# Optimization experiments

Hardware: AMD Instinct MI355X
Metric: run time of the kernel (lower is better)

## Reference

```python
import jax, jax.numpy as jnp
import numpy as np
from jax import lax

WSIZE = 11
SIGMA = 1.5
PAD = WSIZE // 2  # 5
C1 = 0.01 ** 2
C2 = 0.03 ** 2


def _gauss1d():
    x = np.arange(WSIZE) - WSIZE // 2
    g = np.exp(-(x.astype(np.float64) ** 2) / (2.0 * SIGMA ** 2))
    g = g / g.sum()
    return jnp.asarray(g, dtype=jnp.float32)


def _blur3d(x, g):
    """Replicate-pad by 5 on D/H/W then apply the separable 11x11x11 Gaussian.
    x: [N, 1, D, H, W]. Mathematically identical to the dense conv3d in the
    original (the 3D window is an exact outer product of the 1D Gaussian)."""
    xp = jnp.pad(x, ((0, 0), (0, 0), (PAD, PAD), (PAD, PAD), (PAD, PAD)), mode='edge')
    dn = ('NCDHW', 'OIDHW', 'NCDHW')
    for kshape in ((1, 1, WSIZE, 1, 1), (1, 1, 1, WSIZE, 1), (1, 1, 1, 1, WSIZE)):
        xp = lax.conv_general_dilated(xp, g.reshape(kshape), (1, 1, 1), 'VALID',
                                      dimension_numbers=dn)
    return xp


def _rerange(img):
    img = jnp.where(img.max() > 128.0, img / 255.0, img)
    img = jnp.where(img.min() < -0.5, (img + 1.0) / 2.0, img)
    return img


def setup_inputs() -> dict:
    key = jax.random.key(0)
    k1, k2 = jax.random.split(key)
    N, C, H, W = 4, 16, 512, 512
    pred = jax.random.uniform(k1, (N, C, H, W), dtype=jnp.float32)
    gt = jax.random.uniform(k2, (N, C, H, W), dtype=jnp.float32)
    return {"pred": pred, "gt": gt}


def reference(pred, gt):
    N = pred.shape[0]
    pred = _rerange(pred)
    gt = _rerange(gt)

    # ---- PSNR (range = 1.0, reduce='sum') ----
    mse = jnp.mean((pred - gt) ** 2, axis=(1, 2, 3))           # [N]
    psnr = jnp.sum(10.0 * jnp.log10(1.0 / mse))                # scalar

    # ---- 3D SSIM over [N,1,C,H,W] volumes ----
    g = _gauss1d()
    img = pred[:, None]                                        # [N,1,D,H,W]
    gtt = gt[:, None]
    mu1 = _blur3d(img, g)
    mu2 = _blur3d(gtt, g)
    mu1_sq = mu1 * mu1
    mu2_sq = mu2 * mu2
    mu1_mu2 = mu1 * mu2
    sigma1_sq = _blur3d(img * img, g) - mu1_sq
    sigma2_sq = _blur3d(gtt * gtt, g) - mu2_sq
    sigma12 = _blur3d(img * gtt, g) - mu1_mu2

    v1 = 2.0 * sigma12 + C2
    v2 = sigma1_sq + sigma2_sq + C2
    ssim_map = ((2.0 * mu1_mu2 + C1) * v1) / ((mu1_sq + mu2_sq + C1) * v2)
    ssim = jnp.sum(jnp.mean(ssim_map, axis=(1, 2, 3, 4)))      # reduce='sum'

    return psnr, ssim, N
```

## Files before the change

kernel.cpp:

```cpp
#include <hip/hip_runtime.h>
#include <hip/hip_bf16.h>
#include <cmath>


#define NB 4
#define DD 16
#define HH 512
#define WW 512
#define SLICE (HH * WW)
#define VOL (DD * SLICE)
#define C1F 0.0001f
#define C2F 0.0009f

#define TH 16
#define TW 32
#define SH 26
#define SW 42
#define ST 43
#define NTHR 512
#define NIT 3

struct GW { float g[11]; };

__device__ inline float blo(unsigned v) {
  union { unsigned u; float f; } c; c.u = v << 16; return c.f;
}
__device__ inline float bhi(unsigned v) {
  union { unsigned u; float f; } c; c.u = v & 0xFFFF0000u; return c.f;
}
__device__ inline unsigned pack_bf2(float a, float b) {
  __hip_bfloat162 t;
  t.x = __float2bfloat16(a);
  t.y = __float2bfloat16(b);
  union { __hip_bfloat162 h; unsigned u; } c; c.h = t; return c.u;
}

__device__ inline float block_sum512(float v) {
#pragma unroll
  for (int o = 32; o > 0; o >>= 1) v += __shfl_down(v, o, 64);
  __shared__ float r[8];
  if ((threadIdx.x & 63) == 0) r[threadIdx.x >> 6] = v;
  __syncthreads();
  float out = 0.f;
  if (threadIdx.x == 0) {
#pragma unroll
    for (int i = 0; i < 8; ++i) out += r[i];
  }
  __syncthreads();
  return out;
}

__global__ void zero_acc_k(float* acc) {
  if (threadIdx.x < 8) acc[threadIdx.x] = 0.f;
}

__global__ __launch_bounds__(NTHR, 2) void fused_k(
    const float* __restrict__ pred, const float* __restrict__ gt,
    float* __restrict__ acc, GW gw) {
  __shared__ uint2 sd[2][SH * ST];
  __shared__ uint2 tmp[TH * ST];
  __shared__ float WL[DD * DD];
  int b = blockIdx.x;
  int tile = b & 511;
  int n = b >> 9;
  int th0 = (tile >> 4) * TH;
  int tw0 = (tile & 15) * TW;
  int t = threadIdx.x;

  if (t < DD * DD) {
    int dout = t >> 4, d = t & 15;
    float w = 0.f;
#pragma unroll
    for (int k = 0; k < 11; ++k) {
      int j = dout + k - 5; j = j < 0 ? 0 : (j > 15 ? 15 : j);
      if (j == d) w += gw.g[k];
    }
    WL[t] = w;
  }

  int goff[NIT], laddr[NIT];
  bool iv[NIT], own[NIT];
#pragma unroll
  for (int it = 0; it < NIT; ++it) {
    int i = t + it * NTHR;
    iv[it] = i < SH * SW;
    int ii = iv[it] ? i : 0;
    int y = ii / SW, x = ii - y * SW;
    int gy = th0 + y - 5; gy = gy < 0 ? 0 : (gy > HH - 1 ? HH - 1 : gy);
    int gx = tw0 + x - 5; gx = gx < 0 ? 0 : (gx > WW - 1 ? WW - 1 : gx);
    goff[it] = gy * WW + gx;
    laddr[it] = y * ST + x;
    own[it] = (y >= 5) && (y < 5 + TH) && (x >= 5) && (x < 5 + TW);
  }
  const float* pbase = pred + (size_t)n * VOL;
  const float* qbase = gt + (size_t)n * VOL;

  float pv[NIT], qv[NIT];
#pragma unroll
  for (int it = 0; it < NIT; ++it) {
    pv[it] = iv[it] ? pbase[goff[it]] : 0.f;
    qv[it] = iv[it] ? qbase[goff[it]] : 0.f;
  }

  float psnr = 0.f;
  float a0[DD], a1[DD], a2[DD], a3[DD];
#pragma unroll
  for (int j = 0; j < DD; ++j) { a0[j] = a1[j] = a2[j] = a3[j] = 0.f; }
  __syncthreads();

  int wy = t >> 5, wx = t & 31;
#pragma unroll 1
  for (int d = 0; d < DD; ++d) {
    uint2* sdb = sd[d & 1];
#pragma unroll
    for (int it = 0; it < NIT; ++it) {
      if (iv[it]) {
        float S = pv[it] + qv[it], Dm = pv[it] - qv[it];
        sdb[laddr[it]] = make_uint2(pack_bf2(S, Dm), pack_bf2(S * S, Dm * Dm));
        if (own[it]) psnr = fmaf(Dm, Dm, psnr);
      }
    }
    __syncthreads();
    if (d < DD - 1) {
      const float* pd = pbase + (size_t)(d + 1) * SLICE;
      const float* qd = qbase + (size_t)(d + 1) * SLICE;
#pragma unroll
      for (int it = 0; it < NIT; ++it) {
        if (iv[it]) { pv[it] = pd[goff[it]]; qv[it] = qd[goff[it]]; }
      }
    }
    for (int i = t; i < TH * SW; i += NTHR) {
      int r = i / SW, c = i - r * SW;
      float h0 = 0.f, h1 = 0.f, h2 = 0.f, h3 = 0.f;
#pragma unroll
      for (int k = 0; k < 11; ++k) {
        uint2 v = sdb[(r + k) * ST + c];
        float g = gw.g[k];
        h0 = fmaf(g, blo(v.x), h0);
        h1 = fmaf(g, bhi(v.x), h1);
        h2 = fmaf(g, blo(v.y), h2);
        h3 = fmaf(g, bhi(v.y), h3);
      }
      tmp[r * ST + c] = make_uint2(pack_bf2(h0, h1), pack_bf2(h2, h3));
    }
    __syncthreads();
    float w0 = 0.f, w1 = 0.f, w2 = 0.f, w3 = 0.f;
#pragma unroll
    for (int k = 0; k < 11; ++k) {
      uint2 v = tmp[wy * ST + wx + k];
      float g = gw.g[k];
      w0 = fmaf(g, blo(v.x), w0);
      w1 = fmaf(g, bhi(v.x), w1);
      w2 = fmaf(g, blo(v.y), w2);
      w3 = fmaf(g, bhi(v.y), w3);
    }
    const float* wl = WL + d;
#pragma unroll
    for (int dout = 0; dout < DD; ++dout) {
      float w = wl[dout * DD];
      a0[dout] = fmaf(w, w0, a0[dout]);
      a1[dout] = fmaf(w, w1, a1[dout]);
      a2[dout] = fmaf(w, w2, a2[dout]);
      a3[dout] = fmaf(w, w3, a3[dout]);
    }
  }

  float ssum = 0.f;
#pragma unroll
  for (int j = 0; j < DD; ++j) {
    float Sb = a0[j], Db = a1[j], B1 = a2[j], B2 = a3[j];
    float SS = Sb * Sb, DDm = Db * Db;
    float m12_2 = (SS - DDm) * 0.5f;
    float msq   = (SS + DDm) * 0.5f;
    float Epq   = (B1 - B2) * 0.25f;
    float Esum  = (B1 + B2) * 0.5f;
    float sig12_2 = 2.f * Epq - m12_2;
    float svar    = Esum - msq;
    float num = (m12_2 + C1F) * (sig12_2 + C2F);
    float den = (msq + C1F) * (svar + C2F);
    ssum += num / den;
  }
  float bs = block_sum512(ssum);
  if (t == 0) atomicAdd(&acc[4 + n], bs);
  float bp = block_sum512(psnr);
  if (t == 0) atomicAdd(&acc[n], bp);
}

__global__ void final_k(const float* __restrict__ acc, float* __restrict__ out) {
  if (threadIdx.x == 0 && blockIdx.x == 0) {
    double psnr = 0.0, ssim = 0.0;
    for (int n = 0; n < NB; ++n) {
      double mse = (double)acc[n] / (double)VOL;
      psnr += 10.0 * log10(1.0 / mse);
      ssim += (double)acc[4 + n] / (double)VOL;
    }
    out[0] = (float)psnr;
    out[1] = (float)ssim;
    out[2] = (float)NB;
  }
}

extern "C" void kernel_launch(void* const* d_in, const int* in_sizes, int n_in,
                              void* d_out, int out_size, void* d_ws, size_t ws_size,
                              hipStream_t stream) {
  const float* pred = (const float*)d_in[0];
  const float* gt = (const float*)d_in[1];
  float* acc = (float*)d_ws;
  GW gw;
  double tt[11], s = 0.0;
  for (int i = 0; i < 11; ++i) {
    double x = i - 5;
    tt[i] = exp(-(x * x) / 4.5);
    s += tt[i];
  }
  for (int i = 0; i < 11; ++i) gw.g[i] = (float)(tt[i] / s);

  zero_acc_k<<<1, 64, 0, stream>>>(acc);
  fused_k<<<NB * 512, NTHR, 0, stream>>>(pred, gt, acc, gw);
  final_k<<<1, 1, 0, stream>>>(acc, (float*)d_out);
}
```

Baseline: 273.3 us.

## Use packed fp16 dot2 for separable blur with row/column-pair LDS layout

Switches the intermediate blur data from bf16 to fp16 and replaces the scalar FMA taps with v_dot2 instructions over packed pairs of taps. The shared memory is relaid so each word holds two adjacent rows or columns, and the weights are pre-packed on the host as even/odd-phase half2 constants. The depth-mixing weight matrix moves into kernel arguments, which removes the per-block shared-memory setup. The aim is to halve the ALU work and LDS reads in the H and W passes. The cost is fp16 range and precision for the squared terms and more complex indexing.

```diff
diff --git a/kernel.cpp b/kernel.cpp
--- a/kernel.cpp
+++ b/kernel.cpp
@@ -1,5 +1,4 @@
 #include <hip/hip_runtime.h>
-#include <hip/hip_bf16.h>
 #include <cmath>
 
 
@@ -14,25 +13,37 @@
 
 #define TH 16
 #define TW 32
-#define SH 26
 #define SW 42
-#define ST 43
+#define RP 13
+#define CP 21
+#define CPP 22
+#define CPT 22
 #define NTHR 512
-#define NIT 3
-
-struct GW { float g[11]; };
-
-__device__ inline float blo(unsigned v) {
-  union { unsigned u; float f; } c; c.u = v << 16; return c.f;
-}
-__device__ inline float bhi(unsigned v) {
-  union { unsigned u; float f; } c; c.u = v & 0xFFFF0000u; return c.f;
-}
-__device__ inline unsigned pack_bf2(float a, float b) {
-  __hip_bfloat162 t;
-  t.x = __float2bfloat16(a);
-  t.y = __float2bfloat16(b);
-  union { __hip_bfloat162 h; unsigned u; } c; c.h = t; return c.u;
+#define SIT (RP * SW)
+#define HIT (TH * CP)
+#define XTRA (SIT - NTHR)
+
+typedef _Float16 h2v __attribute__((ext_vector_type(2)));
+
+struct KArg {
+  float wlT[DD * DD];
+  unsigned ge[6], go[6];
+};
+
+__device__ inline float dot2h(unsigned a, unsigned b, float c) {
+#if __has_builtin(__builtin_amdgcn_fdot2)
+  return __builtin_amdgcn_fdot2(__builtin_bit_cast(h2v, a),
+                                __builtin_bit_cast(h2v, b), c, false);
+#else
+  h2v av = __builtin_bit_cast(h2v, a), bv = __builtin_bit_cast(h2v, b);
+  return fmaf((float)av.y, (float)bv.y, fmaf((float)av.x, (float)bv.x, c));
+#endif
+}
+__device__ inline unsigned pkh(float a, float b) {
+  return __builtin_bit_cast(unsigned, __builtin_amdgcn_cvt_pkrtz(a, b));
+}
+__device__ inline int iclamp(int v, int lo, int hi) {
+  return v < lo ? lo : (v > hi ? hi : v);
 }
 
 __device__ inline float block_sum512(float v) {
@@ -56,10 +67,12 @@
 
 __global__ __launch_bounds__(NTHR, 2) void fused_k(
     const float* __restrict__ pred, const float* __restrict__ gt,
-    float* __restrict__ acc, GW gw) {
-  __shared__ uint2 sd[2][SH * ST];
-  __shared__ uint2 tmp[TH * ST];
-  __shared__ float WL[DD * DD];
+    float* __restrict__ acc, KArg ka) {
+  __shared__ uint2 sA[2][RP * 2 * CPP];
+  __shared__ uint2 sB[2][RP * 2 * CPP];
+  __shared__ uint2 tA[TH * CPT];
+  __shared__ uint2 tB[TH * CPT];
+
   int b = blockIdx.x;
   int tile = b & 511;
   int n = b >> 9;
@@ -67,97 +80,121 @@
   int tw0 = (tile & 15) * TW;
   int t = threadIdx.x;
 
-  if (t < DD * DD) {
-    int dout = t >> 4, d = t & 15;
-    float w = 0.f;
-#pragma unroll
-    for (int k = 0; k < 11; ++k) {
-      int j = dout + k - 5; j = j < 0 ? 0 : (j > 15 ? 15 : j);
-      if (j == d) w += gw.g[k];
-    }
-    WL[t] = w;
-  }
-
-  int goff[NIT], laddr[NIT];
-  bool iv[NIT], own[NIT];
-#pragma unroll
-  for (int it = 0; it < NIT; ++it) {
-    int i = t + it * NTHR;
-    iv[it] = i < SH * SW;
-    int ii = iv[it] ? i : 0;
-    int y = ii / SW, x = ii - y * SW;
-    int gy = th0 + y - 5; gy = gy < 0 ? 0 : (gy > HH - 1 ? HH - 1 : gy);
-    int gx = tw0 + x - 5; gx = gx < 0 ? 0 : (gx > WW - 1 ? WW - 1 : gx);
-    goff[it] = gy * WW + gx;
-    laddr[it] = y * ST + x;
-    own[it] = (y >= 5) && (y < 5 + TH) && (x >= 5) && (x < 5 + TW);
-  }
-  const float* pbase = pred + (size_t)n * VOL;
-  const float* qbase = gt + (size_t)n * VOL;
-
-  float pv[NIT], qv[NIT];
-#pragma unroll
-  for (int it = 0; it < NIT; ++it) {
-    pv[it] = iv[it] ? pbase[goff[it]] : 0.f;
-    qv[it] = iv[it] ? qbase[goff[it]] : 0.f;
-  }
+  int rpA = t / SW, xA = t - rpA * SW;
+  int r0A = th0 + 2 * rpA - 5;
+  int gxA = iclamp(tw0 + xA - 5, 0, WW - 1);
+  int go00 = iclamp(r0A, 0, HH - 1) * WW + gxA;
+  int go01 = iclamp(r0A + 1, 0, HH - 1) * WW + gxA;
+  int wof0 = (rpA * 2 + (xA & 1)) * CPP + (xA >> 1);
+  bool oxA = (xA >= 5) && (xA < 5 + TW);
+  float o00 = (oxA && rpA >= 3 && rpA <= 10) ? 1.f : 0.f;
+  float o01 = (oxA && rpA >= 2 && rpA <= 9) ? 1.f : 0.f;
+
+  int i1 = t + XTRA;
+  bool has2 = (i1 >= NTHR);
+  int rpB = i1 / SW, xB = i1 - rpB * SW;
+  int r0B = th0 + 2 * rpB - 5;
+  int gxB = iclamp(tw0 + xB - 5, 0, WW - 1);
+  int go10 = iclamp(r0B, 0, HH - 1) * WW + gxB;
+  int go11 = iclamp(r0B + 1, 0, HH - 1) * WW + gxB;
+  int wof1 = (rpB * 2 + (xB & 1)) * CPP + (xB >> 1);
+  bool oxB = (xB >= 5) && (xB < 5 + TW);
+  float o10 = (oxB && rpB >= 3 && rpB <= 10) ? 1.f : 0.f;
+  float o11 = (oxB && rpB >= 2 && rpB <= 9) ? 1.f : 0.f;
+
+  bool hasH = (t < HIT);
+  int hr = t / CP, hcp = t - hr * CP;
+  int hbase = (hr >> 1) * (2 * CPP) + hcp;
+  int htad = hr * CPT + hcp;
+
+  int wy = t >> 5, wx = t & 31;
+  int wbase = wy * CPT + (wx >> 1);
+
+  unsigned ch[6], cw[6];
+#pragma unroll
+  for (int j = 0; j < 6; ++j) {
+    ch[j] = (hr & 1) ? ka.go[j] : ka.ge[j];
+    cw[j] = (wx & 1) ? ka.go[j] : ka.ge[j];
+  }
+
+  const float* pb = pred + (size_t)n * VOL;
+  const float* qb = gt + (size_t)n * VOL;
+
+  float p00 = pb[go00], q00 = qb[go00], p01 = pb[go01], q01 = qb[go01];
+  float p10 = 0.f, q10 = 0.f, p11 = 0.f, q11 = 0.f;
+  if (has2) { p10 = pb[go10]; q10 = qb[go10]; p11 = pb[go11]; q11 = qb[go11]; }
 
   float psnr = 0.f;
   float a0[DD], a1[DD], a2[DD], a3[DD];
 #pragma unroll
   for (int j = 0; j < DD; ++j) { a0[j] = a1[j] = a2[j] = a3[j] = 0.f; }
-  __syncthreads();
-
-  int wy = t >> 5, wx = t & 31;
+
 #pragma unroll 1
   for (int d = 0; d < DD; ++d) {
-    uint2* sdb = sd[d & 1];
-#pragma unroll
-    for (int it = 0; it < NIT; ++it) {
-      if (iv[it]) {
-        float S = pv[it] + qv[it], Dm = pv[it] - qv[it];
-        sdb[laddr[it]] = make_uint2(pack_bf2(S, Dm), pack_bf2(S * S, Dm * Dm));
-        if (own[it]) psnr = fmaf(Dm, Dm, psnr);
+    uint2* sAb = sA[d & 1];
+    uint2* sBb = sB[d & 1];
+    {
+      float S0 = p00 + q00, D0 = p00 - q00;
+      float S1 = p01 + q01, D1 = p01 - q01;
+      float dd0 = D0 * D0, dd1 = D1 * D1;
+      psnr = fmaf(o00, dd0, psnr);
+      psnr = fmaf(o01, dd1, psnr);
+      sAb[wof0] = make_uint2(pkh(S0, S1), pkh(D0, D1));
+      sBb[wof0] = make_uint2(pkh(S0 * S0, S1 * S1), pkh(dd0, dd1));
+    }
+    if (has2) {
+      float S0 = p10 + q10, D0 = p10 - q10;
+      float S1 = p11 + q11, D1 = p11 - q11;
+      float dd0 = D0 * D0, dd1 = D1 * D1;
+      psnr = fmaf(o10, dd0, psnr);
+      psnr = fmaf(o11, dd1, psnr);
+      sAb[wof1] = make_uint2(pkh(S0, S1), pkh(D0, D1));
+      sBb[wof1] = make_uint2(pkh(S0 * S0, S1 * S1), pkh(dd0, dd1));
+    }
+    __syncthreads();
+
+    if (d < DD - 1) {
+      const float* pd = pb + (size_t)(d + 1) * SLICE;
+      const float* qd = qb + (size_t)(d + 1) * SLICE;
+      p00 = pd[go00]; q00 = qd[go00]; p01 = pd[go01]; q01 = qd[go01];
+      if (has2) { p10 = pd[go10]; q10 = qd[go10]; p11 = pd[go11]; q11 = qd[go11]; }
+    }
+
+    if (hasH) {
+      float e0 = 0.f, e1 = 0.f, e2 = 0.f, e3 = 0.f;
+      float f0 = 0.f, f1 = 0.f, f2 = 0.f, f3 = 0.f;
+#pragma unroll
+      for (int j = 0; j < 6; ++j) {
+        uint2 va0 = sAb[hbase + j * (2 * CPP)];
+        uint2 va1 = sAb[hbase + j * (2 * CPP) + CPP];
+        uint2 vb0 = sBb[hbase + j * (2 * CPP)];
+        uint2 vb1 = sBb[hbase + j * (2 * CPP) + CPP];
+        unsigned c = ch[j];
+        e0 = dot2h(c, va0.x, e0); e1 = dot2h(c, va0.y, e1);
+        f0 = dot2h(c, va1.x, f0); f1 = dot2h(c, va1.y, f1);
+        e2 = dot2h(c, vb0.x, e2); e3 = dot2h(c, vb0.y, e3);
+        f2 = dot2h(c, vb1.x, f2); f3 = dot2h(c, vb1.y, f3);
       }
+      tA[htad] = make_uint2(pkh(e0, f0), pkh(e1, f1));
+      tB[htad] = make_uint2(pkh(e2, f2), pkh(e3, f3));
     }
     __syncthreads();
-    if (d < DD - 1) {
-      const float* pd = pbase + (size_t)(d + 1) * SLICE;
-      const float* qd = qbase + (size_t)(d + 1) * SLICE;
-#pragma unroll
-      for (int it = 0; it < NIT; ++it) {
-        if (iv[it]) { pv[it] = pd[goff[it]]; qv[it] = qd[goff[it]]; }
-      }
-    }
-    for (int i = t; i < TH * SW; i += NTHR) {
-      int r = i / SW, c = i - r * SW;
-      float h0 = 0.f, h1 = 0.f, h2 = 0.f, h3 = 0.f;
-#pragma unroll
-      for (int k = 0; k < 11; ++k) {
-        uint2 v = sdb[(r + k) * ST + c];
-        float g = gw.g[k];
-        h0 = fmaf(g, blo(v.x), h0);
-        h1 = fmaf(g, bhi(v.x), h1);
-        h2 = fmaf(g, blo(v.y), h2);
-        h3 = fmaf(g, bhi(v.y), h3);
-      }
-      tmp[r * ST + c] = make_uint2(pack_bf2(h0, h1), pack_bf2(h2, h3));
-    }
-    __syncthreads();
+
     float w0 = 0.f, w1 = 0.f, w2 = 0.f, w3 = 0.f;
 #pragma unroll
-    for (int k = 0; k < 11; ++k) {
-      uint2 v = tmp[wy * ST + wx + k];
-      float g = gw.g[k];
-      w0 = fmaf(g, blo(v.x), w0);
-      w1 = fmaf(g, bhi(v.x), w1);
-      w2 = fmaf(g, blo(v.y), w2);
-      w3 = fmaf(g, bhi(v.y), w3);
-    }
-    const float* wl = WL + d;
+    for (int j = 0; j < 6; ++j) {
+      uint2 va = tA[wbase + j];
+      uint2 vb = tB[wbase + j];
+      unsigned c = cw[j];
+      w0 = dot2h(c, va.x, w0);
+      w1 = dot2h(c, va.y, w1);
+      w2 = dot2h(c, vb.x, w2);
+      w3 = dot2h(c, vb.y, w3);
+    }
+    const float* wl = ka.wlT + d * DD;
 #pragma unroll
     for (int dout = 0; dout < DD; ++dout) {
-      float w = wl[dout * DD];
+      float w = wl[dout];
       a0[dout] = fmaf(w, w0, a0[dout]);
       a1[dout] = fmaf(w, w1, a1[dout]);
       a2[dout] = fmaf(w, w2, a2[dout]);
@@ -200,22 +237,56 @@
   }
 }
 
+static unsigned short f2h(float f) {
+  union { float f; unsigned u; } v; v.f = f;
+  unsigned u = v.u;
+  unsigned s = (u >> 16) & 0x8000u;
+  int e = (int)((u >> 23) & 0xff) - 127 + 15;
+  unsigned m = u & 0x7fffffu;
+  if (e <= 0) return (unsigned short)s;
+  if (e >= 31) return (unsigned short)(s | 0x7c00u);
+  unsigned h = ((unsigned)e << 10) | (m >> 13);
+  unsigned rem = m & 0x1fffu;
+  if (rem > 0x1000u || (rem == 0x1000u && (h & 1u))) h++;
+  return (unsigned short)(s | h);
+}
+
 extern "C" void kernel_launch(void* const* d_in, const int* in_sizes, int n_in,
                               void* d_out, int out_size, void* d_ws, size_t ws_size,
                               hipStream_t stream) {
   const float* pred = (const float*)d_in[0];
   const float* gt = (const float*)d_in[1];
   float* acc = (float*)d_ws;
-  GW gw;
+
   double tt[11], s = 0.0;
   for (int i = 0; i < 11; ++i) {
     double x = i - 5;
     tt[i] = exp(-(x * x) / 4.5);
     s += tt[i];
   }
-  for (int i = 0; i < 11; ++i) gw.g[i] = (float)(tt[i] / s);
+  float g[11];
+  for (int i = 0; i < 11; ++i) g[i] = (float)(tt[i] / s);
+
+  KArg ka;
+  for (int dout = 0; dout < DD; ++dout) {
+    for (int d = 0; d < DD; ++d) {
+      float w = 0.f;
+      for (int k = 0; k < 11; ++k) {
+        int j = dout + k - 5;
+        j = j < 0 ? 0 : (j > 15 ? 15 : j);
+        if (j == d) w += g[k];
+      }
+      ka.wlT[d * DD + dout] = w;
+    }
+  }
+  for (int j = 0; j < 5; ++j)
+    ka.ge[j] = (unsigned)f2h(g[2 * j]) | ((unsigned)f2h(g[2 * j + 1]) << 16);
+  ka.ge[5] = (unsigned)f2h(g[10]);
+  ka.go[0] = ((unsigned)f2h(g[0])) << 16;
+  for (int j = 1; j < 6; ++j)
+    ka.go[j] = (unsigned)f2h(g[2 * j - 1]) | ((unsigned)f2h(g[2 * j]) << 16);
 
   zero_acc_k<<<1, 64, 0, stream>>>(acc);
-  fused_k<<<NB * 512, NTHR, 0, stream>>>(pred, gt, acc, gw);
+  fused_k<<<NB * 512, NTHR, 0, stream>>>(pred, gt, acc, ka);
   final_k<<<1, 1, 0, stream>>>(acc, (float*)d_out);
 }
```

New measurement: 281.7 us. 3.0% more time.
